# Kernel optimization log

Hardware: AMD Instinct MI355X
Metric: run time of the kernel (lower is better)

Reference implementation:

```python
import jax, jax.numpy as jnp
import numpy as np

N_NODES = 50000
N_EDGES = 800000
IN_CH, HID, HEADS, OUT_CH = 16, 64, 4, 8
NEG_SLOPE = 0.2


def _add_self_loops(edge_index, num_nodes):
    loop = jnp.arange(num_nodes, dtype=edge_index.dtype)
    loops = jnp.stack([loop, loop])  # [2, N]
    return jnp.concatenate([edge_index, loops], axis=1)


def _gat_conv(x, src, dst, W, a_src, a_dst, bias, concat):
    """PyG-style GATConv: linear -> per-edge LeakyReLU attention -> segment
    softmax over incoming edges -> scatter-add aggregate."""
    N = x.shape[0]
    H, C = a_src.shape
    h = (x @ W).reshape(N, H, C)                      # [N,H,C]
    alpha_src = (h * a_src).sum(-1)                   # [N,H]
    alpha_dst = (h * a_dst).sum(-1)                   # [N,H]
    e = jax.nn.leaky_relu(alpha_src[src] + alpha_dst[dst], NEG_SLOPE)  # [E,H]
    # numerically stable segment softmax over edges grouped by dst
    e_max = jax.ops.segment_max(e, dst, num_segments=N)
    e_exp = jnp.exp(e - e_max[dst])
    denom = jax.ops.segment_sum(e_exp, dst, num_segments=N)
    alpha = e_exp / denom[dst]                        # [E,H]
    msg = h[src] * alpha[:, :, None]                  # [E,H,C]
    out = jax.ops.segment_sum(msg, dst, num_segments=N)  # [N,H,C]
    if concat:
        return out.reshape(N, H * C) + bias
    return out.mean(axis=1) + bias


def setup_inputs() -> dict:
    key = jax.random.key(0)
    ks = jax.random.split(key, 12)
    s = 0.1
    return {
        "x": jax.random.normal(ks[0], (N_NODES, IN_CH), jnp.float32),
        "edge_index": jax.random.randint(ks[1], (2, N_EDGES), 0, N_NODES, jnp.int64),
        "W1": jax.random.normal(ks[2], (IN_CH, HEADS * HID), jnp.float32) * s,
        "as1": jax.random.normal(ks[3], (HEADS, HID), jnp.float32) * s,
        "ad1": jax.random.normal(ks[4], (HEADS, HID), jnp.float32) * s,
        "b1": jnp.zeros((HEADS * HID,), jnp.float32),
        "W2": jax.random.normal(ks[5], (HEADS * HID, HEADS * HID), jnp.float32) * s,
        "as2": jax.random.normal(ks[6], (HEADS, HID), jnp.float32) * s,
        "ad2": jax.random.normal(ks[7], (HEADS, HID), jnp.float32) * s,
        "b2": jnp.zeros((HID,), jnp.float32),
        "Wc": jax.random.normal(ks[8], (HID, OUT_CH), jnp.float32) * s,
        "bc": jnp.zeros((OUT_CH,), jnp.float32),
    }


def reference(x, edge_index, W1, as1, ad1, b1, W2, as2, ad2, b2, Wc, bc):
    ei = _add_self_loops(edge_index, x.shape[0])
    src, dst = ei[0], ei[1]
    h = _gat_conv(x, src, dst, W1, as1, ad1, b1, concat=True)
    h = jax.nn.elu(h)
    h = _gat_conv(h, src, dst, W2, as2, ad2, b2, concat=False)
    h = jax.nn.elu(h)
    return h @ Wc + bc  # [N, OUT_CH]
```

## Files before the change

kernel.cpp:

```cpp
#include <hip/hip_runtime.h>
#include <math.h>

#define NODES   50000
#define HEADS   4
#define HID     64
#define FDIM    256
#define IN_CH   16
#define NEG_SLOPE 0.2f

typedef unsigned short ushort_t;
typedef unsigned int uint_t;
typedef __attribute__((ext_vector_type(8))) short bf16x8;
typedef __attribute__((ext_vector_type(4))) float f32x4;
typedef __attribute__((ext_vector_type(2))) float f32x2;

__device__ inline ushort_t f2bf(float f) {
    uint_t u = __float_as_uint(f);
    u += 0x7fffu + ((u >> 16) & 1u);
    return (ushort_t)(u >> 16);
}
__device__ inline uint_t f2h(float f) {
    _Float16 h = (_Float16)f;
    return (uint_t)*(ushort_t*)&h;
}
__device__ inline float h2f(uint_t u) {
    ushort_t us = (ushort_t)u;
    _Float16 h = *(_Float16*)&us;
    return (float)h;
}


__global__ __launch_bounds__(256) void k_prep(const float* __restrict__ x,
                                              const float* __restrict__ W1,
                                              const float* __restrict__ as1,
                                              const float* __restrict__ ad1,
                                              const float* __restrict__ W2,
                                              const int* __restrict__ ei, int E,
                                              ushort_t* __restrict__ h,
                                              float* __restrict__ asrc,
                                              float* __restrict__ adst,
                                              ushort_t* __restrict__ W2T,
                                              int* __restrict__ deg, int Nn, int NB) {
    int bid = blockIdx.x, t = threadIdx.x;
    if (bid >= NB + 256) {
        int e = (bid - NB - 256) * 256 + t;
        int Etot = E + Nn;
        if (e >= Etot) return;
        int d = (e < E) ? ei[E + e] : (e - E);
        if (d >= 0 && d < Nn) atomicAdd(&deg[d], 1);
        return;
    }
    if (bid >= NB) {
        int idx = (bid - NB) * 256 + t;
        int n = idx >> 8, k = idx & 255;
        W2T[idx] = f2bf(W2[k * FDIM + n]);
        return;
    }
    float w1c[16];
#pragma unroll
    for (int k = 0; k < 16; ++k) w1c[k] = W1[k * FDIM + t];
    float av = as1[t], dv = ad1[t];
    int hh = t >> 6;
#pragma unroll
    for (int j = 0; j < 8; ++j) {
        int n = bid * 8 + j;
        if (n >= Nn) break;
        const float4* xp = (const float4*)(x + n * IN_CH);
        float4 x0 = xp[0], x1 = xp[1], x2 = xp[2], x3 = xp[3];
        float s = x0.x * w1c[0]  + x0.y * w1c[1]  + x0.z * w1c[2]  + x0.w * w1c[3]
                + x1.x * w1c[4]  + x1.y * w1c[5]  + x1.z * w1c[6]  + x1.w * w1c[7]
                + x2.x * w1c[8]  + x2.y * w1c[9]  + x2.z * w1c[10] + x2.w * w1c[11]
                + x3.x * w1c[12] + x3.y * w1c[13] + x3.z * w1c[14] + x3.w * w1c[15];
        uint_t pv = (uint_t)f2bf(s);
        uint_t ov = __shfl_down(pv, 1);
        if (!(t & 1)) *(uint_t*)(h + (long)n * FDIM + t) = pv | (ov << 16);
        float p1 = s * av, p2 = s * dv;
#pragma unroll
        for (int off = 1; off < 64; off <<= 1) {
            p1 += __shfl_xor(p1, off);
            p2 += __shfl_xor(p2, off);
        }
        if ((t & 63) == 0) {
            asrc[n * 4 + hh] = p1;
            adst[n * 4 + hh] = p2;
        }
    }
}


__global__ __launch_bounds__(256) void k_scanA(const int* __restrict__ deg,
                                               int* __restrict__ bsum, int N) {
    __shared__ int sh[256];
    int t = threadIdx.x;
    int i0 = blockIdx.x * 4096 + t * 16;
    int s = 0;
#pragma unroll
    for (int j = 0; j < 16; ++j) s += (i0 + j < N) ? deg[i0 + j] : 0;
    sh[t] = s;
    __syncthreads();
    for (int off = 128; off; off >>= 1) {
        if (t < off) sh[t] += sh[t + off];
        __syncthreads();
    }
    if (t == 0) bsum[blockIdx.x] = sh[0];
}

__global__ __launch_bounds__(256) void k_scanC(const int* __restrict__ deg,
                                               const int* __restrict__ bsum,
                                               int* __restrict__ rowst,
                                               int* __restrict__ cursor, int N, int nb) {
    __shared__ int sh[256];
    __shared__ int boff[64];
    int t = threadIdx.x, b = blockIdx.x;
    if (t < 64) {
        int orig = (t < nb) ? bsum[t] : 0;
        int v = orig;
#pragma unroll
        for (int off = 1; off < 64; off <<= 1) {
            int u = __shfl_up(v, off);
            if (t >= off) v += u;
        }
        boff[t] = v - orig;
        if (t == 63 && b == 0) rowst[N] = v;
    }
    int i0 = b * 4096 + t * 16;
    int v[16], s = 0;
#pragma unroll
    for (int j = 0; j < 16; ++j) { v[j] = (i0 + j < N) ? deg[i0 + j] : 0; s += v[j]; }
    sh[t] = s;
    __syncthreads();
    for (int off = 1; off < 256; off <<= 1) {
        int u = (t >= off) ? sh[t - off] : 0;
        __syncthreads();
        sh[t] += u;
        __syncthreads();
    }
    int excl = sh[t] - s + boff[b];
#pragma unroll
    for (int j = 0; j < 16; ++j) {
        if (i0 + j < N) { rowst[i0 + j] = excl; cursor[i0 + j] = excl; }
        excl += v[j];
    }
}


__global__ void k_scatter(const int* __restrict__ ei, int E, int N,
                          int* __restrict__ cursor, int2* __restrict__ csr2) {
    int e = blockIdx.x * blockDim.x + threadIdx.x;
    int Etot = E + N;
    if (e >= Etot) return;
    int s, d;
    if (e < E) { s = ei[e]; d = ei[E + e]; } else { s = d = e - E; }
    if (d < 0 || d >= N) return;
    int pos = atomicAdd(&cursor[d], 1);
    csr2[pos] = make_int2(s, d);
}


__global__ __launch_bounds__(256) void k_gemm2(const ushort_t* __restrict__ A,
                                               const ushort_t* __restrict__ BT,
                                               const float* __restrict__ as2,
                                               const float* __restrict__ ad2,
                                               ushort_t* __restrict__ C,
                                               float* __restrict__ asrc,
                                               float* __restrict__ adst, int M) {
    __shared__ short As[64 * 40];
    __shared__ short Bs[64 * 40];
    __shared__ float2 red[64][2];
    int tid = threadIdx.x;
    int row0 = blockIdx.y * 64, col0 = blockIdx.x * 64;
    int wid = tid >> 6, lane = tid & 63;
    int wm = wid >> 1, wn = wid & 1;
    int quad = lane >> 4, lm = lane & 15;
    int lr = tid >> 2, lk = (tid & 3) * 8;
    f32x4 acc[2][2] = {};
    for (int k0 = 0; k0 < FDIM; k0 += 32) {
        uint4 av = {0u, 0u, 0u, 0u};
        int ar = row0 + lr;
        if (ar < M) av = *(const uint4*)(A + (long)ar * FDIM + k0 + lk);
        *(uint4*)(&As[lr * 40 + lk]) = av;
        uint4 bv = *(const uint4*)(BT + (long)(col0 + lr) * FDIM + k0 + lk);
        *(uint4*)(&Bs[lr * 40 + lk]) = bv;
        __syncthreads();
        bf16x8 a0 = *(const bf16x8*)(&As[(wm * 32 + lm) * 40 + quad * 8]);
        bf16x8 a1 = *(const bf16x8*)(&As[(wm * 32 + 16 + lm) * 40 + quad * 8]);
        bf16x8 b0 = *(const bf16x8*)(&Bs[(wn * 32 + lm) * 40 + quad * 8]);
        bf16x8 b1 = *(const bf16x8*)(&Bs[(wn * 32 + 16 + lm) * 40 + quad * 8]);
        acc[0][0] = __builtin_amdgcn_mfma_f32_16x16x32_bf16(a0, b0, acc[0][0], 0, 0, 0);
        acc[0][1] = __builtin_amdgcn_mfma_f32_16x16x32_bf16(a0, b1, acc[0][1], 0, 0, 0);
        acc[1][0] = __builtin_amdgcn_mfma_f32_16x16x32_bf16(a1, b0, acc[1][0], 0, 0, 0);
        acc[1][1] = __builtin_amdgcn_mfma_f32_16x16x32_bf16(a1, b1, acc[1][1], 0, 0, 0);
        __syncthreads();
    }
#pragma unroll
    for (int mi = 0; mi < 2; ++mi)
#pragma unroll
        for (int ni = 0; ni < 2; ++ni)
#pragma unroll
            for (int r = 0; r < 4; ++r) {
                int row = row0 + wm * 32 + mi * 16 + quad * 4 + r;
                int col = col0 + wn * 32 + ni * 16 + lm;
                if (row < M) C[(long)row * FDIM + col] = f2bf(acc[mi][ni][r]);
            }
    float asv0 = as2[col0 + wn * 32 + lm], asv1 = as2[col0 + wn * 32 + 16 + lm];
    float adv0 = ad2[col0 + wn * 32 + lm], adv1 = ad2[col0 + wn * 32 + 16 + lm];
#pragma unroll
    for (int mi = 0; mi < 2; ++mi)
#pragma unroll
        for (int r = 0; r < 4; ++r) {
            float ps = acc[mi][0][r] * asv0 + acc[mi][1][r] * asv1;
            float pd = acc[mi][0][r] * adv0 + acc[mi][1][r] * adv1;
#pragma unroll
            for (int off = 1; off < 16; off <<= 1) {
                ps += __shfl_xor(ps, off);
                pd += __shfl_xor(pd, off);
            }
            if (lm == 0) red[wm * 32 + mi * 16 + quad * 4 + r][wn] = make_float2(ps, pd);
        }
    __syncthreads();
    if (tid < 64) {
        int row = row0 + tid;
        if (row < M) {
            float2 e0 = red[tid][0], e1 = red[tid][1];
            asrc[row * 4 + blockIdx.x] = e0.x + e1.x;
            adst[row * 4 + blockIdx.x] = e0.y + e1.y;
        }
    }
}


__global__ void k_pw(const int2* __restrict__ csr2, const float* __restrict__ asrc,
                     const float* __restrict__ adst, uint_t* __restrict__ pwb, int Etot) {
    int e = blockIdx.x * blockDim.x + threadIdx.x;
    if (e >= Etot) return;
    int2 sd = csr2[e];
    float4 av = *(const float4*)(asrc + sd.x * 4);
    float4 dv = *(const float4*)(adst + sd.y * 4);
    float t[4] = {av.x + dv.x, av.y + dv.y, av.z + dv.z, av.w + dv.w};
    uint_t sh = (uint_t)sd.x << 16;
#pragma unroll
    for (int h = 0; h < 4; ++h) {
        float tt = (t[h] > 0.f) ? t[h] : NEG_SLOPE * t[h];
        pwb[h * Etot + e] = sh | f2h(__expf(tt));
    }
}


__device__ inline void fma8(f32x2& a0, f32x2& a1, f32x2& a2, f32x2& a3,
                            uint4 hv, float pw) {
    f32x2 p = {pw, pw};
    f32x2 u;
    u.x = __uint_as_float(hv.x << 16); u.y = __uint_as_float(hv.x & 0xffff0000u);
    a0 += p * u;
    u.x = __uint_as_float(hv.y << 16); u.y = __uint_as_float(hv.y & 0xffff0000u);
    a1 += p * u;
    u.x = __uint_as_float(hv.z << 16); u.y = __uint_as_float(hv.z & 0xffff0000u);
    a2 += p * u;
    u.x = __uint_as_float(hv.w << 16); u.y = __uint_as_float(hv.w & 0xffff0000u);
    a3 += p * u;
}

__global__ __launch_bounds__(256) void k_agg(const ushort_t* __restrict__ h,
                                             const uint_t* __restrict__ pwb,
                                             const int* __restrict__ row_start,
                                             const float* __restrict__ b1,
                                             const float* __restrict__ b2,
                                             const float* __restrict__ Wc,
                                             const float* __restrict__ bc,
                                             ushort_t* __restrict__ hout,
                                             float* __restrict__ fout,
                                             int mode, int Etot, int N) {
    __shared__ float zsh[2 * FDIM];
    __shared__ float wsh[584];
    int tid  = threadIdx.x;
    int hh   = tid >> 6;
    int lane = tid & 63;
    int half = lane >> 5;
    int l32  = lane & 31;
    int g    = l32 >> 3;
    int cg   = l32 & 7;
    int d    = blockIdx.x * 2 + half;
    bool valid = d < N;

    if (!mode) {
        for (int i = tid; i < 584; i += 256)
            wsh[i] = (i < 512) ? Wc[i] : ((i < 520) ? bc[i - 512] : b2[i - 520]);
    }

    int s0 = 0, s1 = 0;
    if (valid) { s0 = row_start[d]; s1 = row_start[d + 1]; }
    int cnt  = s1 - s0;
    int maxc = max(cnt, __shfl_xor(cnt, 32));
    const uint_t* pwp = pwb + (long)hh * Etot;
    const char* hbase = (const char*)h + (hh * HID + cg * 8) * 2;

    f32x2 a0 = {0.f, 0.f}, a1 = {0.f, 0.f}, a2 = {0.f, 0.f}, a3 = {0.f, 0.f};
    float den = 0.f;

    for (int off = 0; off < maxc; off += 16) {
        int i0 = s0 + off + g;
        uint_t u0 = (i0      < s1) ? pwp[i0]      : 0u;
        uint_t u1 = (i0 + 4  < s1) ? pwp[i0 + 4]  : 0u;
        uint_t u2 = (i0 + 8  < s1) ? pwp[i0 + 8]  : 0u;
        uint_t u3 = (i0 + 12 < s1) ? pwp[i0 + 12] : 0u;
        uint4 hv0 = *(const uint4*)(hbase + ((size_t)(u0 >> 16) << 9));
        uint4 hv1 = *(const uint4*)(hbase + ((size_t)(u1 >> 16) << 9));
        uint4 hv2 = *(const uint4*)(hbase + ((size_t)(u2 >> 16) << 9));
        uint4 hv3 = *(const uint4*)(hbase + ((size_t)(u3 >> 16) << 9));
        float pw0 = h2f(u0 & 0xffffu), pw1 = h2f(u1 & 0xffffu);
        float pw2 = h2f(u2 & 0xffffu), pw3 = h2f(u3 & 0xffffu);
        den += (pw0 + pw1) + (pw2 + pw3);
        fma8(a0, a1, a2, a3, hv0, pw0);
        fma8(a0, a1, a2, a3, hv1, pw1);
        fma8(a0, a1, a2, a3, hv2, pw2);
        fma8(a0, a1, a2, a3, hv3, pw3);
    }
#pragma unroll
    for (int o = 8; o <= 16; o <<= 1) {
        a0.x += __shfl_xor(a0.x, o); a0.y += __shfl_xor(a0.y, o);
        a1.x += __shfl_xor(a1.x, o); a1.y += __shfl_xor(a1.y, o);
        a2.x += __shfl_xor(a2.x, o); a2.y += __shfl_xor(a2.y, o);
        a3.x += __shfl_xor(a3.x, o); a3.y += __shfl_xor(a3.y, o);
        den  += __shfl_xor(den, o);
    }

    if (mode) {
        if (g == 0 && valid) {
            float inv = 1.f / den;
            float v[8] = {a0.x, a0.y, a1.x, a1.y, a2.x, a2.y, a3.x, a3.y};
            const float* bp = b1 + hh * HID + cg * 8;
#pragma unroll
            for (int j = 0; j < 8; ++j) {
                float t = v[j] * inv + bp[j];
                v[j] = (t > 0.f) ? t : __expf(t) - 1.f;
            }
            uint4 u;
            u.x = (uint_t)f2bf(v[0]) | ((uint_t)f2bf(v[1]) << 16);
            u.y = (uint_t)f2bf(v[2]) | ((uint_t)f2bf(v[3]) << 16);
            u.z = (uint_t)f2bf(v[4]) | ((uint_t)f2bf(v[5]) << 16);
            u.w = (uint_t)f2bf(v[6]) | ((uint_t)f2bf(v[7]) << 16);
            *(uint4*)(hout + (long)d * FDIM + hh * HID + cg * 8) = u;
        }
    } else {
        if (g == 0 && valid) {
            float inv = 1.f / den;
            float v[8] = {a0.x, a0.y, a1.x, a1.y, a2.x, a2.y, a3.x, a3.y};
            int zb = half * FDIM + hh * HID + cg * 8;
#pragma unroll
            for (int j = 0; j < 8; ++j) zsh[zb + j] = v[j] * inv;
        }
        __syncthreads();
        if (tid < 128) {
            int node = tid >> 6, c = tid & 63;
            int dd = blockIdx.x * 2 + node;
            if (dd < N) {
                const float* zp = zsh + node * FDIM;
                float zv = 0.25f * (zp[c] + zp[64 + c] + zp[128 + c] + zp[192 + c])
                         + wsh[520 + c];
                zv = (zv > 0.f) ? zv : __expf(zv) - 1.f;
                zsh[node * FDIM + c] = zv;
            }
        }
        __syncthreads();
        if (tid < 16) {
            int node = tid >> 3, o = tid & 7;
            int dd = blockIdx.x * 2 + node;
            if (dd < N) {
                float acc = wsh[512 + o];
                const float* zp = zsh + node * FDIM;
#pragma unroll 8
                for (int c = 0; c < 64; ++c) acc += zp[c] * wsh[c * 8 + o];
                fout[(long)dd * 8 + o] = acc;
            }
        }
    }
}


extern "C" void kernel_launch(void* const* d_in, const int* in_sizes, int n_in,
                              void* d_out, int out_size, void* d_ws, size_t ws_size,
                              hipStream_t stream) {
    const float* x   = (const float*)d_in[0];
    const int*   ei  = (const int*)d_in[1];
    const float* W1  = (const float*)d_in[2];
    const float* as1 = (const float*)d_in[3];
    const float* ad1 = (const float*)d_in[4];
    const float* b1  = (const float*)d_in[5];
    const float* W2  = (const float*)d_in[6];
    const float* as2 = (const float*)d_in[7];
    const float* ad2 = (const float*)d_in[8];
    const float* b2  = (const float*)d_in[9];
    const float* Wc  = (const float*)d_in[10];
    const float* bc  = (const float*)d_in[11];
    float* out = (float*)d_out;

    const int N = NODES;
    const int E = in_sizes[1] / 2;
    const int Etot = E + N;

    char* ws = (char*)d_ws;
    size_t off = 0;
    auto alloc = [&](size_t bytes) {
        void* p = ws + off;
        off = (off + bytes + 255) & ~(size_t)255;
        return p;
    };
    ushort_t* hbf    = (ushort_t*)alloc((size_t)N * FDIM * 2);
    ushort_t* hact   = (ushort_t*)alloc((size_t)N * FDIM * 2);
    float*    asrc   = (float*)alloc((size_t)N * HEADS * 4);
    float*    adst   = (float*)alloc((size_t)N * HEADS * 4);
    ushort_t* W2T    = (ushort_t*)alloc((size_t)FDIM * FDIM * 2);
    int*      deg    = (int*)alloc((size_t)N * 4);
    int*      rowst  = (int*)alloc((size_t)(N + 1) * 4);
    int*      cursor = (int*)alloc((size_t)N * 4);
    int*      bsum   = (int*)alloc(64 * 4);
    int2*     csr2   = (int2*)alloc((size_t)Etot * 8);
    uint_t*   pwb    = (uint_t*)alloc((size_t)Etot * HEADS * 4);

    const int tpb = 256;
    int egrid = (Etot + tpb - 1) / tpb;
    int nb = (N + 4095) / 4096;
    int NB = (N + 7) / 8;

    hipMemsetAsync(deg, 0, (size_t)N * 4, stream);

    k_prep<<<NB + 256 + egrid, tpb, 0, stream>>>(x, W1, as1, ad1, W2, ei, E,
                                                 hbf, asrc, adst, W2T, deg, N, NB);
    k_scanA<<<nb, 256, 0, stream>>>(deg, bsum, N);
    k_scanC<<<nb, 256, 0, stream>>>(deg, bsum, rowst, cursor, N, nb);
    k_scatter<<<egrid, tpb, 0, stream>>>(ei, E, N, cursor, csr2);

    k_pw<<<egrid, tpb, 0, stream>>>(csr2, asrc, adst, pwb, Etot);
    k_agg<<<(N + 1) / 2, 256, 0, stream>>>(hbf, pwb, rowst, b1, nullptr, nullptr, nullptr,
                                           hact, nullptr, 1, Etot, N);

    dim3 g2(FDIM / 64, (N + 63) / 64);
    k_gemm2<<<g2, 256, 0, stream>>>(hact, W2T, as2, ad2, hbf, asrc, adst, N);
    k_pw<<<egrid, tpb, 0, stream>>>(csr2, asrc, adst, pwb, Etot);
    k_agg<<<(N + 1) / 2, 256, 0, stream>>>(hbf, pwb, rowst, nullptr, b2, Wc, bc,
                                           nullptr, out, 0, Etot, N);
}
```

Baseline: 386.7 us.

## Store only CSR sources, recover dst via rowstart search, interleave per-edge head weights

The scatter now writes only the source index per edge, halving CSR storage. k_pw recovers each edge's destination by binary-searching row_start, first globally per block and then within a shared-memory window. The per-edge attention weights for the four heads are written as one 16-byte record instead of four separate head-major arrays. k_agg indexes that interleaved layout, trading contiguous per-head loads for strided 4-byte reads within each 16-byte record. This adds the binary-search cost in k_pw.

```diff
diff --git a/kernel.cpp b/kernel.cpp
--- a/kernel.cpp
+++ b/kernel.cpp
@@ -145,7 +145,7 @@
 
 
 __global__ void k_scatter(const int* __restrict__ ei, int E, int N,
-                          int* __restrict__ cursor, int2* __restrict__ csr2) {
+                          int* __restrict__ cursor, int* __restrict__ csr) {
     int e = blockIdx.x * blockDim.x + threadIdx.x;
     int Etot = E + N;
     if (e >= Etot) return;
@@ -153,7 +153,7 @@
     if (e < E) { s = ei[e]; d = ei[E + e]; } else { s = d = e - E; }
     if (d < 0 || d >= N) return;
     int pos = atomicAdd(&cursor[d], 1);
-    csr2[pos] = make_int2(s, d);
+    csr[pos] = s;
 }
 
 
@@ -229,20 +229,56 @@
 }
 
 
-__global__ void k_pw(const int2* __restrict__ csr2, const float* __restrict__ asrc,
-                     const float* __restrict__ adst, uint_t* __restrict__ pwb, int Etot) {
-    int e = blockIdx.x * blockDim.x + threadIdx.x;
+__global__ __launch_bounds__(256) void k_pw(const int* __restrict__ csr,
+                                            const int* __restrict__ rowst,
+                                            const float* __restrict__ asrc,
+                                            const float* __restrict__ adst,
+                                            uint4* __restrict__ pwb4,
+                                            int Etot, int N) {
+    __shared__ int rsh[257];
+    __shared__ int dlo_s;
+    int t = threadIdx.x;
+    int e0 = blockIdx.x * 256;
+    if (t == 0) {
+        int lo = 0, hi = N;
+        while (hi - lo > 1) {
+            int mid = (lo + hi) >> 1;
+            if (rowst[mid] <= e0) lo = mid; else hi = mid;
+        }
+        dlo_s = lo;
+    }
+    __syncthreads();
+    int dlo = dlo_s;
+    int i = dlo + t;
+    rsh[t] = (i <= N) ? rowst[i] : (Etot + 1);
+    if (t == 0) {
+        int i2 = dlo + 256;
+        rsh[256] = (i2 <= N) ? rowst[i2] : (Etot + 1);
+    }
+    __syncthreads();
+    int e = e0 + t;
     if (e >= Etot) return;
-    int2 sd = csr2[e];
-    float4 av = *(const float4*)(asrc + sd.x * 4);
-    float4 dv = *(const float4*)(adst + sd.y * 4);
-    float t[4] = {av.x + dv.x, av.y + dv.y, av.z + dv.z, av.w + dv.w};
-    uint_t sh = (uint_t)sd.x << 16;
-#pragma unroll
-    for (int h = 0; h < 4; ++h) {
-        float tt = (t[h] > 0.f) ? t[h] : NEG_SLOPE * t[h];
-        pwb[h * Etot + e] = sh | f2h(__expf(tt));
-    }
+    int lo = 0, hi = 257;
+    while (hi - lo > 1) {
+        int mid = (lo + hi) >> 1;
+        if (rsh[mid] <= e) lo = mid; else hi = mid;
+    }
+    int d = dlo + lo;
+    int s = csr[e];
+    float4 av = *(const float4*)(asrc + s * 4);
+    float4 dv = *(const float4*)(adst + d * 4);
+    float tt[4] = {av.x + dv.x, av.y + dv.y, av.z + dv.z, av.w + dv.w};
+    uint_t sh = (uint_t)s << 16;
+    uint4 o;
+    float v0 = (tt[0] > 0.f) ? tt[0] : NEG_SLOPE * tt[0];
+    float v1 = (tt[1] > 0.f) ? tt[1] : NEG_SLOPE * tt[1];
+    float v2 = (tt[2] > 0.f) ? tt[2] : NEG_SLOPE * tt[2];
+    float v3 = (tt[3] > 0.f) ? tt[3] : NEG_SLOPE * tt[3];
+    o.x = sh | f2h(__expf(v0));
+    o.y = sh | f2h(__expf(v1));
+    o.z = sh | f2h(__expf(v2));
+    o.w = sh | f2h(__expf(v3));
+    pwb4[e] = o;
 }
 
 
@@ -269,7 +305,7 @@
                                              const float* __restrict__ bc,
                                              ushort_t* __restrict__ hout,
                                              float* __restrict__ fout,
-                                             int mode, int Etot, int N) {
+                                             int mode, int N) {
     __shared__ float zsh[2 * FDIM];
     __shared__ float wsh[584];
     int tid  = threadIdx.x;
@@ -291,7 +327,6 @@
     if (valid) { s0 = row_start[d]; s1 = row_start[d + 1]; }
     int cnt  = s1 - s0;
     int maxc = max(cnt, __shfl_xor(cnt, 32));
-    const uint_t* pwp = pwb + (long)hh * Etot;
     const char* hbase = (const char*)h + (hh * HID + cg * 8) * 2;
 
     f32x2 a0 = {0.f, 0.f}, a1 = {0.f, 0.f}, a2 = {0.f, 0.f}, a3 = {0.f, 0.f};
@@ -299,10 +334,10 @@
 
     for (int off = 0; off < maxc; off += 16) {
         int i0 = s0 + off + g;
-        uint_t u0 = (i0      < s1) ? pwp[i0]      : 0u;
-        uint_t u1 = (i0 + 4  < s1) ? pwp[i0 + 4]  : 0u;
-        uint_t u2 = (i0 + 8  < s1) ? pwp[i0 + 8]  : 0u;
-        uint_t u3 = (i0 + 12 < s1) ? pwp[i0 + 12] : 0u;
+        uint_t u0 = (i0      < s1) ? pwb[((i0)      << 2) + hh] : 0u;
+        uint_t u1 = (i0 + 4  < s1) ? pwb[((i0 + 4)  << 2) + hh] : 0u;
+        uint_t u2 = (i0 + 8  < s1) ? pwb[((i0 + 8)  << 2) + hh] : 0u;
+        uint_t u3 = (i0 + 12 < s1) ? pwb[((i0 + 12) << 2) + hh] : 0u;
         uint4 hv0 = *(const uint4*)(hbase + ((size_t)(u0 >> 16) << 9));
         uint4 hv1 = *(const uint4*)(hbase + ((size_t)(u1 >> 16) << 9));
         uint4 hv2 = *(const uint4*)(hbase + ((size_t)(u2 >> 16) << 9));
@@ -414,8 +449,8 @@
     int*      rowst  = (int*)alloc((size_t)(N + 1) * 4);
     int*      cursor = (int*)alloc((size_t)N * 4);
     int*      bsum   = (int*)alloc(64 * 4);
-    int2*     csr2   = (int2*)alloc((size_t)Etot * 8);
-    uint_t*   pwb    = (uint_t*)alloc((size_t)Etot * HEADS * 4);
+    int*      csr    = (int*)alloc((size_t)Etot * 4);
+    uint4*    pwb4   = (uint4*)alloc((size_t)Etot * 16);
 
     const int tpb = 256;
     int egrid = (Etot + tpb - 1) / tpb;
@@ -428,15 +463,16 @@
                                                  hbf, asrc, adst, W2T, deg, N, NB);
     k_scanA<<<nb, 256, 0, stream>>>(deg, bsum, N);
     k_scanC<<<nb, 256, 0, stream>>>(deg, bsum, rowst, cursor, N, nb);
-    k_scatter<<<egrid, tpb, 0, stream>>>(ei, E, N, cursor, csr2);
-
-    k_pw<<<egrid, tpb, 0, stream>>>(csr2, asrc, adst, pwb, Etot);
-    k_agg<<<(N + 1) / 2, 256, 0, stream>>>(hbf, pwb, rowst, b1, nullptr, nullptr, nullptr,
-                                           hact, nullptr, 1, Etot, N);
+    k_scatter<<<egrid, tpb, 0, stream>>>(ei, E, N, cursor, csr);
+
+    k_pw<<<egrid, tpb, 0, stream>>>(csr, rowst, asrc, adst, pwb4, Etot, N);
+    k_agg<<<(N + 1) / 2, 256, 0, stream>>>(hbf, (const uint_t*)pwb4, rowst, b1,
+                                           nullptr, nullptr, nullptr,
+                                           hact, nullptr, 1, N);
 
     dim3 g2(FDIM / 64, (N + 63) / 64);
     k_gemm2<<<g2, 256, 0, stream>>>(hact, W2T, as2, ad2, hbf, asrc, adst, N);
-    k_pw<<<egrid, tpb, 0, stream>>>(csr2, asrc, adst, pwb, Etot);
-    k_agg<<<(N + 1) / 2, 256, 0, stream>>>(hbf, pwb, rowst, nullptr, b2, Wc, bc,
-                                           nullptr, out, 0, Etot, N);
-}
+    k_pw<<<egrid, tpb, 0, stream>>>(csr, rowst, asrc, adst, pwb4, Etot, N);
+    k_agg<<<(N + 1) / 2, 256, 0, stream>>>(hbf, (const uint_t*)pwb4, rowst, nullptr,
+                                           b2, Wc, bc, nullptr, out, 0, N);
+}
```

Result: no change. 393.3 us (+1.7%).
